# Kernel optimization log

Hardware: AMD Instinct MI355X
Metric: run time of the kernel (lower is better)

Reference implementation:

```python
import jax, jax.numpy as jnp
import numpy as np

D_MODEL = 1024
N_HEAD = 16
HEAD_DIM = D_MODEL // N_HEAD


def setup_inputs() -> dict:
    key = jax.random.key(0)
    ks = jax.random.split(key, 5)
    B, T = 2, 2048
    s = 1.0 / np.sqrt(D_MODEL)
    return {
        "x": jax.random.normal(ks[0], (B, T, D_MODEL), dtype=jnp.float32),
        "w_qkv": jax.random.normal(ks[1], (D_MODEL, 3 * D_MODEL), dtype=jnp.float32) * s,
        "b_qkv": jnp.zeros((3 * D_MODEL,), dtype=jnp.float32),
        "w_proj": jax.random.normal(ks[2], (D_MODEL, D_MODEL), dtype=jnp.float32) * s,
        "b_proj": jnp.zeros((D_MODEL,), dtype=jnp.float32),
    }


def reference(x, w_qkv, b_qkv, w_proj, b_proj):
    B, T, C = x.shape
    H, Dh = N_HEAD, HEAD_DIM
    scale = Dh ** -0.5
    qkv = x @ w_qkv + b_qkv                      # [B,T,3C]
    q, k, v = jnp.split(qkv, 3, axis=2)
    # [B,T,C] -> [B,H,T,Dh]
    q = q.reshape(B, T, H, Dh).transpose(0, 2, 1, 3)
    k = k.reshape(B, T, H, Dh).transpose(0, 2, 1, 3)
    v = v.reshape(B, T, H, Dh).transpose(0, 2, 1, 3)
    att = jnp.einsum("bhqd,bhkd->bhqk", q, k) * scale  # [B,H,T,T]
    causal = jnp.tril(jnp.ones((T, T), dtype=bool))
    att = jnp.where(causal, att, -jnp.inf)
    att = jax.nn.softmax(att, axis=-1)
    out = jnp.einsum("bhqk,bhkd->bhqd", att, v)  # [B,H,T,Dh]
    out = out.transpose(0, 2, 1, 3).reshape(B, T, C)
    return out @ w_proj + b_proj
```

## Files before the change

### kernel.cpp

```cpp
#include <hip/hip_runtime.h>
#include <hip/hip_bf16.h>

#define B_ 2
#define T_ 2048
#define C_ 1024
#define H_ 16
#define DH_ 64

typedef __attribute__((ext_vector_type(8))) short bf16x8;
typedef __attribute__((ext_vector_type(4))) float f32x4;
typedef __attribute__((ext_vector_type(4))) unsigned int u32x4;

#define DEVI static __device__ __forceinline__

DEVI unsigned short f2bf(float f) {
  unsigned int u = __float_as_uint(f);
  u = (u + 0x7fffu + ((u >> 16) & 1u)) >> 16;
  return (unsigned short)u;
}

DEVI f32x4 mfma16(bf16x8 a, bf16x8 b, f32x4 c) {
  return __builtin_amdgcn_mfma_f32_16x16x32_bf16(a, b, c, 0, 0, 0);
}

DEVI void gload_lds16(const unsigned short* g, unsigned short* l) {
  __builtin_amdgcn_global_load_lds(
      (const __attribute__((address_space(1))) unsigned int*)g,
      (__attribute__((address_space(3))) unsigned int*)l, 16, 0, 0);
}

DEVI unsigned int cvtpk_bf16(float lo, float hi) {
  unsigned int r;
  asm("v_cvt_pk_bf16_f32 %0, %1, %2" : "=v"(r) : "v"(lo), "v"(hi));
  return r;
}

DEVI int kperm(int kv) {
  return (kv & 3) | (((kv >> 3) & 1) << 2) | (((kv >> 5) & 1) << 3) |
         (((kv >> 2) & 1) << 4) | (((kv >> 4) & 1) << 5);
}

__global__ __launch_bounds__(256) void prep_kernel(
    const float* __restrict__ x, const float* __restrict__ w_qkv,
    const float* __restrict__ w_proj, unsigned short* __restrict__ xb,
    unsigned short* __restrict__ wqkvT, unsigned short* __restrict__ wprojT) {
  __shared__ float tile[32][33];
  int b = blockIdx.x, tid = threadIdx.x;
  if (b < 4096) {
    int i = b * 256 + tid;
    float4 v = reinterpret_cast<const float4*>(x)[i];
    ushort4 o;
    o.x = f2bf(v.x); o.y = f2bf(v.y); o.z = f2bf(v.z); o.w = f2bf(v.w);
    reinterpret_cast<ushort4*>(xb)[i] = o;
  } else {
    const float* in;
    unsigned short* out;
    int R, C, bb;
    if (b < 7168) { bb = b - 4096; in = w_qkv; out = wqkvT; R = 1024; C = 3072; }
    else          { bb = b - 7168; in = w_proj; out = wprojT; R = 1024; C = 1024; }
    int nbx = C >> 5;
    int c0 = (bb % nbx) * 32, r0 = (bb / nbx) * 32;
    int tx = tid & 31, ty = tid >> 5;
#pragma unroll
    for (int j = 0; j < 32; j += 8)
      tile[ty + j][tx] = in[(size_t)(r0 + ty + j) * C + c0 + tx];
    __syncthreads();
#pragma unroll
    for (int j = 0; j < 32; j += 8)
      out[(size_t)(c0 + ty + j) * R + r0 + tx] = f2bf(tile[tx][ty + j]);
  }
}

__global__ __launch_bounds__(256, 2) void gemm192_qkv(
    const unsigned short* __restrict__ A, const unsigned short* __restrict__ Bt,
    const float* __restrict__ bias,
    unsigned short* __restrict__ qbuf, unsigned short* __restrict__ kbuf,
    unsigned short* __restrict__ vtbuf) {
  __shared__ __attribute__((aligned(16))) unsigned short As[2][128 * 64];
  __shared__ __attribute__((aligned(16))) unsigned short Bs[2][192 * 64];
  const int Kd = 1024;
  int tid = threadIdx.x;
  int lane = tid & 63, w = tid >> 6;
  int wn = w;
  int lrow = lane & 15, lgrp = lane >> 4;

  int g = blockIdx.x;
  int gs = (g & 7) * 64 + (g >> 3);
  int by = gs >> 4, bx = gs & 15;
  int bm = by * 128, bn = bx * 192;
  const unsigned short* Ab = A + (size_t)bm * Kd;
  const unsigned short* Bb = Bt + (size_t)bn * Kd;

  int sL[2], scl[2];
#pragma unroll
  for (int it = 0; it < 2; ++it) {
    int c = tid + it * 256;
    int L = c >> 3, s = c & 7, v = s ^ (L & 7);
    sL[it] = L;
    scl[it] = (v >> 2) * 32 + (v & 3) * 8;
  }

  auto stgA = [&](int t, int h) {
    unsigned short* dst = As[t & 1] + h * 4096;
    int k0 = t << 6;
#pragma unroll
    for (int it = 0; it < 2; ++it)
      gload_lds16(Ab + (size_t)(h * 64 + sL[it]) * Kd + k0 + scl[it],
                  dst + (tid + it * 256) * 8);
  };
  auto stgB3 = [&](int t, int th) {
    unsigned short* dst = Bs[t & 1] + th * 4096;
    int k0 = t << 6;
#pragma unroll
    for (int it = 0; it < 2; ++it)
      gload_lds16(Bb + (size_t)(th * 64 + sL[it]) * Kd + k0 + scl[it],
                  dst + (tid + it * 256) * 8);
  };

  auto lda = [&](const unsigned short* buf, int mi, int kk) -> bf16x8 {
    int row = mi * 16 + lrow;
    int s = ((kk << 2) | lgrp) ^ (row & 7);
    return *reinterpret_cast<const bf16x8*>((const char*)buf + row * 128 + s * 16);
  };
  auto ldb = [&](const unsigned short* buf, int ni, int kk) -> bf16x8 {
    int row = wn * 48 + ni * 16 + lrow;
    int s = ((kk << 2) | lgrp) ^ (row & 7);
    return *reinterpret_cast<const bf16x8*>((const char*)buf + row * 128 + s * 16);
  };

  f32x4 acc[8][3] = {};
  bf16x8 bfr[3][2], af[2][2];

#define PHASE_TAIL                                          \
  __builtin_amdgcn_s_barrier();                             \
  __builtin_amdgcn_s_setprio(1);

#define MFMA_TRI(base)                                      \
  _Pragma("unroll") for (int ii = 0; ii < 2; ++ii)          \
  _Pragma("unroll") for (int ni = 0; ni < 3; ++ni) {        \
    acc[(base) + ii][ni] = mfma16(af[ii][0], bfr[ni][0], acc[(base) + ii][ni]); \
    acc[(base) + ii][ni] = mfma16(af[ii][1], bfr[ni][1], acc[(base) + ii][ni]); \
  }

#define PHASE_END                                           \
  __builtin_amdgcn_s_setprio(0);                            \
  __builtin_amdgcn_s_barrier();

  stgA(0, 0); stgA(0, 1);
  stgB3(0, 0); stgB3(0, 1); stgB3(0, 2);
  stgB3(1, 0); stgB3(1, 1); stgB3(1, 2);
  asm volatile("s_waitcnt vmcnt(6)" ::: "memory");
  __builtin_amdgcn_s_barrier();

#pragma unroll 1
  for (int j = 0; j < 8; ++j) {
    const bool nl = (j < 7);
    const int t1 = 2 * j + 1, t2 = 2 * j + 2, t3 = 2 * j + 3;

#pragma unroll
    for (int ni = 0; ni < 3; ++ni) { bfr[ni][0] = ldb(Bs[0], ni, 0); bfr[ni][1] = ldb(Bs[0], ni, 1); }
    af[0][0] = lda(As[0], 0, 0); af[0][1] = lda(As[0], 0, 1);
    af[1][0] = lda(As[0], 1, 0); af[1][1] = lda(As[0], 1, 1);
    stgA(t1, 0);
    PHASE_TAIL; MFMA_TRI(0); PHASE_END;

    af[0][0] = lda(As[0], 2, 0); af[0][1] = lda(As[0], 2, 1);
    af[1][0] = lda(As[0], 3, 0); af[1][1] = lda(As[0], 3, 1);
    stgA(t1, 1);
    if (nl) stgB3(t2, 0);
    PHASE_TAIL; MFMA_TRI(2); PHASE_END;

    af[0][0] = lda(As[0], 4, 0); af[0][1] = lda(As[0], 4, 1);
    af[1][0] = lda(As[0], 5, 0); af[1][1] = lda(As[0], 5, 1);
    if (nl) stgB3(t2, 1);
    PHASE_TAIL; MFMA_TRI(4); PHASE_END;

    af[0][0] = lda(As[0], 6, 0); af[0][1] = lda(As[0], 6, 1);
    af[1][0] = lda(As[0], 7, 0); af[1][1] = lda(As[0], 7, 1);
    if (nl) stgB3(t2, 2);
    PHASE_TAIL; MFMA_TRI(6);
    __builtin_amdgcn_s_setprio(0);
    if (nl) { asm volatile("s_waitcnt vmcnt(6)" ::: "memory"); }
    else    { asm volatile("s_waitcnt vmcnt(0)" ::: "memory"); }
    __builtin_amdgcn_s_barrier();

#pragma unroll
    for (int ni = 0; ni < 3; ++ni) { bfr[ni][0] = ldb(Bs[1], ni, 0); bfr[ni][1] = ldb(Bs[1], ni, 1); }
    af[0][0] = lda(As[1], 0, 0); af[0][1] = lda(As[1], 0, 1);
    af[1][0] = lda(As[1], 1, 0); af[1][1] = lda(As[1], 1, 1);
    if (nl) stgA(t2, 0);
    PHASE_TAIL; MFMA_TRI(0); PHASE_END;

    af[0][0] = lda(As[1], 2, 0); af[0][1] = lda(As[1], 2, 1);
    af[1][0] = lda(As[1], 3, 0); af[1][1] = lda(As[1], 3, 1);
    if (nl) { stgA(t2, 1); stgB3(t3, 0); }
    PHASE_TAIL; MFMA_TRI(2); PHASE_END;

    af[0][0] = lda(As[1], 4, 0); af[0][1] = lda(As[1], 4, 1);
    af[1][0] = lda(As[1], 5, 0); af[1][1] = lda(As[1], 5, 1);
    if (nl) stgB3(t3, 1);
    PHASE_TAIL; MFMA_TRI(4); PHASE_END;

    af[0][0] = lda(As[1], 6, 0); af[0][1] = lda(As[1], 6, 1);
    af[1][0] = lda(As[1], 7, 0); af[1][1] = lda(As[1], 7, 1);
    if (nl) stgB3(t3, 2);
    PHASE_TAIL; MFMA_TRI(6);
    __builtin_amdgcn_s_setprio(0);
    if (nl) { asm volatile("s_waitcnt vmcnt(6)" ::: "memory"); }
    __builtin_amdgcn_s_barrier();
  }
#undef PHASE_TAIL
#undef MFMA_TRI
#undef PHASE_END

  int c0 = bn + wn * 48;
#pragma unroll
  for (int ni = 0; ni < 3; ++ni) {
    int col = c0 + ni * 16 + lrow;
    float bv = bias[col];
    int which = col >> 10, cc = col & 1023;
    int h = cc >> 6, d = cc & 63;
#pragma unroll
    for (int mi = 0; mi < 8; ++mi) {
      int rowb = bm + mi * 16 + lgrp * 4;
      int b = rowb >> 11, tt = rowb & 2047;
      if (which == 2) {
        ushort4 pk;
        pk.x = f2bf(acc[mi][ni][0] + bv);
        pk.y = f2bf(acc[mi][ni][1] + bv);
        pk.z = f2bf(acc[mi][ni][2] + bv);
        pk.w = f2bf(acc[mi][ni][3] + bv);
        *reinterpret_cast<ushort4*>(vtbuf + ((size_t)((b * 16 + h) * 64 + d)) * T_ + tt) = pk;
      } else {
        unsigned short* dst = (which == 0) ? qbuf : kbuf;
        size_t base = ((size_t)(b * 16 + h) * T_ + tt) * DH_ + d;
#pragma unroll
        for (int r = 0; r < 4; ++r)
          dst[base + (size_t)r * DH_] = f2bf(acc[mi][ni][r] + bv);
      }
    }
  }
}

__global__ __launch_bounds__(256, 2) void gemm_proj(
    const unsigned short* __restrict__ A, const unsigned short* __restrict__ Bt,
    const float* __restrict__ bias, float* __restrict__ outp) {
  __shared__ __attribute__((aligned(16))) unsigned short As[2][128 * 64];
  __shared__ __attribute__((aligned(16))) unsigned short Bs[2][128 * 64];
  const int Kd = 1024, Nd = 1024;
  int tid = threadIdx.x;
  int lane = tid & 63, w = tid >> 6;
  int wn = w;
  int lrow = lane & 15, lgrp = lane >> 4;

  int g = blockIdx.x;
  int gs = (g & 7) * 32 + (g >> 3);
  int by = gs >> 3, bx = gs & 7;
  int bm = by * 128, bn = bx * 128;
  const unsigned short* Ab = A + (size_t)bm * Kd;
  const unsigned short* Bb = Bt + (size_t)bn * Kd;

  int sL[2], scl[2];
#pragma unroll
  for (int it = 0; it < 2; ++it) {
    int c = tid + it * 256;
    int L = c >> 3, s = c & 7, v = s ^ (L & 7);
    sL[it] = L;
    scl[it] = (v >> 2) * 32 + (v & 3) * 8;
  }

  auto stgA = [&](int t, int h) {
    unsigned short* dst = As[t & 1] + h * 4096;
    int k0 = t << 6;
#pragma unroll
    for (int it = 0; it < 2; ++it)
      gload_lds16(Ab + (size_t)(h * 64 + sL[it]) * Kd + k0 + scl[it],
                  dst + (tid + it * 256) * 8);
  };
  auto stgB = [&](int t, int h) {
    unsigned short* dst = Bs[t & 1] + h * 4096;
    int k0 = t << 6;
#pragma unroll
    for (int it = 0; it < 2; ++it)
      gload_lds16(Bb + (size_t)(h * 64 + sL[it]) * Kd + k0 + scl[it],
                  dst + (tid + it * 256) * 8);
  };

  auto lda = [&](const unsigned short* buf, int mi, int kk) -> bf16x8 {
    int row = mi * 16 + lrow;
    int s = ((kk << 2) | lgrp) ^ (row & 7);
    return *reinterpret_cast<const bf16x8*>((const char*)buf + row * 128 + s * 16);
  };
  auto ldb = [&](const unsigned short* buf, int ni, int kk) -> bf16x8 {
    int row = wn * 32 + ni * 16 + lrow;
    int s = ((kk << 2) | lgrp) ^ (row & 7);
    return *reinterpret_cast<const bf16x8*>((const char*)buf + row * 128 + s * 16);
  };

  f32x4 acc[8][2] = {};
  bf16x8 bfr[2][2], af[2][2];

#define PHASE_TAIL                                          \
  __builtin_amdgcn_s_barrier();                             \
  __builtin_amdgcn_s_setprio(1);

#define MFMA_DUO(base)                                      \
  _Pragma("unroll") for (int ii = 0; ii < 2; ++ii)          \
  _Pragma("unroll") for (int ni = 0; ni < 2; ++ni) {        \
    acc[(base) + ii][ni] = mfma16(af[ii][0], bfr[ni][0], acc[(base) + ii][ni]); \
    acc[(base) + ii][ni] = mfma16(af[ii][1], bfr[ni][1], acc[(base) + ii][ni]); \
  }

#define PHASE_END                                           \
  __builtin_amdgcn_s_setprio(0);                            \
  __builtin_amdgcn_s_barrier();

  stgA(0, 0); stgA(0, 1); stgB(0, 0); stgB(0, 1);
  stgB(1, 0); stgB(1, 1);
  asm volatile("s_waitcnt vmcnt(4)" ::: "memory");
  __builtin_amdgcn_s_barrier();

#pragma unroll 1
  for (int j = 0; j < 8; ++j) {
    const bool nl = (j < 7);
    const int t1 = 2 * j + 1, t2 = 2 * j + 2, t3 = 2 * j + 3;

#pragma unroll
    for (int ni = 0; ni < 2; ++ni) { bfr[ni][0] = ldb(Bs[0], ni, 0); bfr[ni][1] = ldb(Bs[0], ni, 1); }
    af[0][0] = lda(As[0], 0, 0); af[0][1] = lda(As[0], 0, 1);
    af[1][0] = lda(As[0], 1, 0); af[1][1] = lda(As[0], 1, 1);
    stgA(t1, 0);
    PHASE_TAIL; MFMA_DUO(0); PHASE_END;

    af[0][0] = lda(As[0], 2, 0); af[0][1] = lda(As[0], 2, 1);
    af[1][0] = lda(As[0], 3, 0); af[1][1] = lda(As[0], 3, 1);
    stgA(t1, 1);
    if (nl) stgB(t2, 0);
    PHASE_TAIL; MFMA_DUO(2); PHASE_END;

    af[0][0] = lda(As[0], 4, 0); af[0][1] = lda(As[0], 4, 1);
    af[1][0] = lda(As[0], 5, 0); af[1][1] = lda(As[0], 5, 1);
    if (nl) stgB(t2, 1);
    PHASE_TAIL; MFMA_DUO(4); PHASE_END;

    af[0][0] = lda(As[0], 6, 0); af[0][1] = lda(As[0], 6, 1);
    af[1][0] = lda(As[0], 7, 0); af[1][1] = lda(As[0], 7, 1);
    PHASE_TAIL; MFMA_DUO(6);
    __builtin_amdgcn_s_setprio(0);
    if (nl) { asm volatile("s_waitcnt vmcnt(4)" ::: "memory"); }
    else    { asm volatile("s_waitcnt vmcnt(0)" ::: "memory"); }
    __builtin_amdgcn_s_barrier();

#pragma unroll
    for (int ni = 0; ni < 2; ++ni) { bfr[ni][0] = ldb(Bs[1], ni, 0); bfr[ni][1] = ldb(Bs[1], ni, 1); }
    af[0][0] = lda(As[1], 0, 0); af[0][1] = lda(As[1], 0, 1);
    af[1][0] = lda(As[1], 1, 0); af[1][1] = lda(As[1], 1, 1);
    if (nl) stgA(t2, 0);
    PHASE_TAIL; MFMA_DUO(0); PHASE_END;

    af[0][0] = lda(As[1], 2, 0); af[0][1] = lda(As[1], 2, 1);
    af[1][0] = lda(As[1], 3, 0); af[1][1] = lda(As[1], 3, 1);
    if (nl) { stgA(t2, 1); stgB(t3, 0); }
    PHASE_TAIL; MFMA_DUO(2); PHASE_END;

    af[0][0] = lda(As[1], 4, 0); af[0][1] = lda(As[1], 4, 1);
    af[1][0] = lda(As[1], 5, 0); af[1][1] = lda(As[1], 5, 1);
    if (nl) stgB(t3, 1);
    PHASE_TAIL; MFMA_DUO(4); PHASE_END;

    af[0][0] = lda(As[1], 6, 0); af[0][1] = lda(As[1], 6, 1);
    af[1][0] = lda(As[1], 7, 0); af[1][1] = lda(As[1], 7, 1);
    PHASE_TAIL; MFMA_DUO(6);
    __builtin_amdgcn_s_setprio(0);
    if (nl) { asm volatile("s_waitcnt vmcnt(4)" ::: "memory"); }
    __builtin_amdgcn_s_barrier();
  }
#undef PHASE_TAIL
#undef MFMA_DUO
#undef PHASE_END

  int c0 = bn + wn * 32;
#pragma unroll
  for (int ni = 0; ni < 2; ++ni) {
    int col = c0 + ni * 16 + lrow;
    float bv = bias[col];
#pragma unroll
    for (int mi = 0; mi < 8; ++mi) {
      int rowb = bm + mi * 16 + lgrp * 4;
#pragma unroll
      for (int r = 0; r < 4; ++r)
        outp[(size_t)(rowb + r) * Nd + col] = acc[mi][ni][r] + bv;
    }
  }
}

__global__ __launch_bounds__(256, 4) void attn_kernel(
    const unsigned short* __restrict__ qbuf,
    const unsigned short* __restrict__ kbuf,
    const unsigned short* __restrict__ vtbuf,
    unsigned short* __restrict__ attno) {
  __shared__ __attribute__((aligned(16))) unsigned short Ks[64 * 64];
  __shared__ __attribute__((aligned(16))) unsigned short Vts[64 * 64];

  int tid = threadIdx.x;
  int lane = tid & 63, w = tid >> 6;
  int lrow = lane & 15, lgrp = lane >> 4;

  int g = blockIdx.x;
  int s = g >> 8;
  int p = (g >> 3) & 7;
  int bh = (g & 7) | (((g >> 6) & 3) << 3);
  int qb = (s == 0) ? p : (s == 1) ? (31 - p) : (s == 2) ? (8 + p) : (23 - p);
  int wq0 = qb * 64 + w * 16;
  int nkb = qb + 1;

  const unsigned short* Qb = qbuf + (size_t)bh * T_ * DH_;
  const unsigned short* Kb = kbuf + (size_t)bh * T_ * DH_;
  const unsigned short* Vb = vtbuf + (size_t)bh * DH_ * T_;

  int srow0 = tid >> 3, scol = tid & 7;
  int srow1 = srow0 + 32;
  int pk0 = kperm(srow0), pk1 = kperm(srow1);
  int soffK0 = pk0 * 128 + ((scol * 16) ^ ((pk0 & 7) << 4));
  int soffK1 = pk1 * 128 + ((scol * 16) ^ ((pk1 & 7) << 4));
  int soffV0 = srow0 * 128 + ((scol * 16) ^ ((srow0 & 7) << 4));
  int soffV1 = srow1 * 128 + ((scol * 16) ^ ((srow1 & 7) << 4));

  const float SC = 0.125f * 1.44269504f;
  int kvbase = ((lgrp & 1) << 3) | ((lgrp >> 1) << 5);
  const int koff[4] = {0, 4, 16, 20};

  bf16x8 qf[2];
#pragma unroll
  for (int ks = 0; ks < 2; ++ks)
    qf[ks] = *reinterpret_cast<const bf16x8*>(
        Qb + (size_t)(wq0 + lrow) * DH_ + ks * 32 + lgrp * 8);

  f32x4 o[4] = {};
  float l_run = 0.f;

  bf16x8 sk0, sk1, sv0, sv1;
  auto stage_load = [&](int kb) {
    sk0 = *reinterpret_cast<const bf16x8*>(Kb + (size_t)(kb * 64 + srow0) * DH_ + scol * 8);
    sk1 = *reinterpret_cast<const bf16x8*>(Kb + (size_t)(kb * 64 + srow1) * DH_ + scol * 8);
    sv0 = *reinterpret_cast<const bf16x8*>(Vb + (size_t)srow0 * T_ + kb * 64 + scol * 8);
    sv1 = *reinterpret_cast<const bf16x8*>(Vb + (size_t)srow1 * T_ + kb * 64 + scol * 8);
  };
  auto stage_write = [&]() {
    *reinterpret_cast<bf16x8*>((char*)Ks + soffK0) = sk0;
    *reinterpret_cast<bf16x8*>((char*)Ks + soffK1) = sk1;
    *reinterpret_cast<bf16x8*>((char*)Vts + soffV0) = sv0;
    *reinterpret_cast<bf16x8*>((char*)Vts + soffV1) = sv1;
  };

  stage_load(0);
#pragma unroll 1
  for (int kb = 0; kb < nkb; ++kb) {
    if (kb > 0) __syncthreads();
    stage_write();
    __syncthreads();
    if (kb + 1 < nkb) stage_load(kb + 1);

    f32x4 sreg[4] = {};
#pragma unroll
    for (int ks = 0; ks < 2; ++ks) {
      bf16x8 kf[4];
#pragma unroll
      for (int ni = 0; ni < 4; ++ni) {
        int kr = ni * 16 + lrow;
        int off = kr * 128 + (((ks * 32 + lgrp * 8) * 2) ^ ((kr & 7) << 4));
        kf[ni] = *reinterpret_cast<const bf16x8*>((const char*)Ks + off);
      }
      __builtin_amdgcn_s_setprio(1);
#pragma unroll
      for (int ni = 0; ni < 4; ++ni)
        sreg[ni] = mfma16(kf[ni], qf[ks], sreg[ni]);
      __builtin_amdgcn_s_setprio(0);
    }

    if (kb == qb) {
      int q = wq0 + lrow;
#pragma unroll
      for (int ni = 0; ni < 4; ++ni) {
        int kvb = kb * 64 + kvbase + koff[ni];
#pragma unroll
        for (int r = 0; r < 4; ++r)
          if (kvb + r > q) sreg[ni][r] = -1e30f;
      }
    }

    f32x4 e[4];
#pragma unroll
    for (int ni = 0; ni < 4; ++ni)
#pragma unroll
      for (int r = 0; r < 4; ++r)
        e[ni][r] = __builtin_amdgcn_exp2f(sreg[ni][r] * SC);

    f32x4 ts = (e[0] + e[1]) + (e[2] + e[3]);
    l_run += (ts[0] + ts[1]) + (ts[2] + ts[3]);

    unsigned int Aw[4], Bw[4];
    Aw[0] = cvtpk_bf16(e[0][0], e[0][1]); Aw[1] = cvtpk_bf16(e[0][2], e[0][3]);
    Aw[2] = cvtpk_bf16(e[1][0], e[1][1]); Aw[3] = cvtpk_bf16(e[1][2], e[1][3]);
    Bw[0] = cvtpk_bf16(e[2][0], e[2][1]); Bw[1] = cvtpk_bf16(e[2][2], e[2][3]);
    Bw[2] = cvtpk_bf16(e[3][0], e[3][1]); Bw[3] = cvtpk_bf16(e[3][2], e[3][3]);
    u32x4 p0v, p1v;
#pragma unroll
    for (int ww = 0; ww < 4; ++ww) {
      auto sw = __builtin_amdgcn_permlane32_swap(Aw[ww], Bw[ww], false, false);
      p0v[ww] = sw[0];
      p1v[ww] = sw[1];
    }
    bf16x8 pa[2];
    pa[0] = __builtin_bit_cast(bf16x8, p0v);
    pa[1] = __builtin_bit_cast(bf16x8, p1v);

#pragma unroll
    for (int ks = 0; ks < 2; ++ks) {
      bf16x8 vf[4];
#pragma unroll
      for (int di = 0; di < 4; ++di) {
        int vr = di * 16 + lrow;
        int off = vr * 128 + (((ks * 32 + lgrp * 8) * 2) ^ ((vr & 7) << 4));
        vf[di] = *reinterpret_cast<const bf16x8*>((const char*)Vts + off);
      }
      __builtin_amdgcn_s_setprio(1);
#pragma unroll
      for (int di = 0; di < 4; ++di)
        o[di] = mfma16(pa[ks], vf[di], o[di]);
      __builtin_amdgcn_s_setprio(0);
    }
  }

  float rs = l_run;
  rs += __shfl_xor(rs, 16);
  rs += __shfl_xor(rs, 32);
  float linv = 1.0f / rs;

  int b = bh >> 4, h = bh & 15;
  float lr[4];
#pragma unroll
  for (int r = 0; r < 4; ++r) lr[r] = __shfl(linv, lgrp * 4 + r);
#pragma unroll
  for (int r = 0; r < 4; ++r) {
    int q = wq0 + lgrp * 4 + r;
    size_t base = ((size_t)(b * T_ + q)) * C_ + h * 64 + lrow;
#pragma unroll
    for (int di = 0; di < 4; ++di)
      attno[base + (size_t)di * 16] = f2bf(o[di][r] * lr[r]);
  }
}

extern "C" void kernel_launch(void* const* d_in, const int* in_sizes, int n_in,
                              void* d_out, int out_size, void* d_ws, size_t ws_size,
                              hipStream_t stream) {
  const float* x      = (const float*)d_in[0];
  const float* w_qkv  = (const float*)d_in[1];
  const float* b_qkv  = (const float*)d_in[2];
  const float* w_proj = (const float*)d_in[3];
  const float* b_proj = (const float*)d_in[4];

  char* ws = (char*)d_ws;
  unsigned short* xb     = (unsigned short*)(ws + 0);
  unsigned short* wqkvT  = (unsigned short*)(ws + 8388608);
  unsigned short* wprojT = (unsigned short*)(ws + 14680064);
  unsigned short* qbuf   = (unsigned short*)(ws + 16777216);
  unsigned short* kbuf   = (unsigned short*)(ws + 25165824);
  unsigned short* vtbuf  = (unsigned short*)(ws + 33554432);
  unsigned short* attno  = (unsigned short*)(ws + 41943040);

  prep_kernel<<<8192, 256, 0, stream>>>(x, w_qkv, w_proj, xb, wqkvT, wprojT);
  gemm192_qkv<<<dim3(512), 256, 0, stream>>>(xb, wqkvT, b_qkv, qbuf, kbuf, vtbuf);
  attn_kernel<<<dim3(1024), 256, 0, stream>>>(qbuf, kbuf, vtbuf, attno);
  gemm_proj<<<dim3(256), 256, 0, stream>>>(attno, wprojT, b_proj, (float*)d_out);
}
```

Before: 91.89 us.

## Double-buffer attention K/V tiles with direct global-to-LDS loads

The attention kernel now stages K and V tiles straight into shared memory with global_load_lds, with source addresses chosen so the existing swizzle and K permutation land correctly. Two LDS buffers let the next tile load while the current one is computed. This drops the register round trip and one barrier per iteration. In exchange LDS use doubles, which may limit occupancy under the 4-blocks launch bound, and the inverse-permutation addressing must be exact.

```diff
diff --git a/kernel.cpp b/kernel.cpp
--- a/kernel.cpp
+++ b/kernel.cpp
@@ -38,6 +38,10 @@
 DEVI int kperm(int kv) {
   return (kv & 3) | (((kv >> 3) & 1) << 2) | (((kv >> 5) & 1) << 3) |
          (((kv >> 2) & 1) << 4) | (((kv >> 4) & 1) << 5);
+}
+DEVI int kperm_inv(int R) {
+  return (R & 3) | (((R >> 4) & 1) << 2) | (((R >> 2) & 1) << 3) |
+         (((R >> 5) & 1) << 4) | (((R >> 3) & 1) << 5);
 }
 
 __global__ __launch_bounds__(256) void prep_kernel(
@@ -399,8 +403,8 @@
     const unsigned short* __restrict__ kbuf,
     const unsigned short* __restrict__ vtbuf,
     unsigned short* __restrict__ attno) {
-  __shared__ __attribute__((aligned(16))) unsigned short Ks[64 * 64];
-  __shared__ __attribute__((aligned(16))) unsigned short Vts[64 * 64];
+  __shared__ __attribute__((aligned(16))) unsigned short Ks[2][64 * 64];
+  __shared__ __attribute__((aligned(16))) unsigned short Vts[2][64 * 64];
 
   int tid = threadIdx.x;
   int lane = tid & 63, w = tid >> 6;
@@ -418,13 +422,15 @@
   const unsigned short* Kb = kbuf + (size_t)bh * T_ * DH_;
   const unsigned short* Vb = vtbuf + (size_t)bh * DH_ * T_;
 
-  int srow0 = tid >> 3, scol = tid & 7;
-  int srow1 = srow0 + 32;
-  int pk0 = kperm(srow0), pk1 = kperm(srow1);
-  int soffK0 = pk0 * 128 + ((scol * 16) ^ ((pk0 & 7) << 4));
-  int soffK1 = pk1 * 128 + ((scol * 16) ^ ((pk1 & 7) << 4));
-  int soffV0 = srow0 * 128 + ((scol * 16) ^ ((srow0 & 7) << 4));
-  int soffV1 = srow1 * 128 + ((scol * 16) ^ ((srow1 & 7) << 4));
+  int kgo[2], vgo[2], cdst[2];
+#pragma unroll
+  for (int it = 0; it < 2; ++it) {
+    int c = w * 128 + it * 64 + lane;
+    int R = c >> 3, sw = c & 7;
+    kgo[it] = kperm_inv(R) * DH_ + (sw ^ (R & 7)) * 8;
+    vgo[it] = R * T_ + (sw ^ (R & 7)) * 8;
+    cdst[it] = c * 8;
+  }
 
   const float SC = 0.125f * 1.44269504f;
   int kvbase = ((lgrp & 1) << 3) | ((lgrp >> 1) << 5);
@@ -439,27 +445,24 @@
   f32x4 o[4] = {};
   float l_run = 0.f;
 
-  bf16x8 sk0, sk1, sv0, sv1;
-  auto stage_load = [&](int kb) {
-    sk0 = *reinterpret_cast<const bf16x8*>(Kb + (size_t)(kb * 64 + srow0) * DH_ + scol * 8);
-    sk1 = *reinterpret_cast<const bf16x8*>(Kb + (size_t)(kb * 64 + srow1) * DH_ + scol * 8);
-    sv0 = *reinterpret_cast<const bf16x8*>(Vb + (size_t)srow0 * T_ + kb * 64 + scol * 8);
-    sv1 = *reinterpret_cast<const bf16x8*>(Vb + (size_t)srow1 * T_ + kb * 64 + scol * 8);
-  };
-  auto stage_write = [&]() {
-    *reinterpret_cast<bf16x8*>((char*)Ks + soffK0) = sk0;
-    *reinterpret_cast<bf16x8*>((char*)Ks + soffK1) = sk1;
-    *reinterpret_cast<bf16x8*>((char*)Vts + soffV0) = sv0;
-    *reinterpret_cast<bf16x8*>((char*)Vts + soffV1) = sv1;
-  };
-
-  stage_load(0);
+  auto stage_issue = [&](int kb, int buf) {
+#pragma unroll
+    for (int it = 0; it < 2; ++it) {
+      gload_lds16(Kb + (size_t)kb * 64 * DH_ + kgo[it], Ks[buf] + cdst[it]);
+      gload_lds16(Vb + (size_t)kb * 64 + vgo[it], Vts[buf] + cdst[it]);
+    }
+  };
+
+  stage_issue(0, 0);
 #pragma unroll 1
   for (int kb = 0; kb < nkb; ++kb) {
-    if (kb > 0) __syncthreads();
-    stage_write();
+    int cur = kb & 1;
+    asm volatile("s_waitcnt vmcnt(0)" ::: "memory");
     __syncthreads();
-    if (kb + 1 < nkb) stage_load(kb + 1);
+    if (kb + 1 < nkb) stage_issue(kb + 1, cur ^ 1);
+
+    const char* kbase = (const char*)Ks[cur];
+    const char* vbase = (const char*)Vts[cur];
 
     f32x4 sreg[4] = {};
 #pragma unroll
@@ -469,7 +472,7 @@
       for (int ni = 0; ni < 4; ++ni) {
         int kr = ni * 16 + lrow;
         int off = kr * 128 + (((ks * 32 + lgrp * 8) * 2) ^ ((kr & 7) << 4));
-        kf[ni] = *reinterpret_cast<const bf16x8*>((const char*)Ks + off);
+        kf[ni] = *reinterpret_cast<const bf16x8*>(kbase + off);
       }
       __builtin_amdgcn_s_setprio(1);
 #pragma unroll
@@ -522,7 +525,7 @@
       for (int di = 0; di < 4; ++di) {
         int vr = di * 16 + lrow;
         int off = vr * 128 + (((ks * 32 + lgrp * 8) * 2) ^ ((vr & 7) << 4));
-        vf[di] = *reinterpret_cast<const bf16x8*>((const char*)Vts + off);
+        vf[di] = *reinterpret_cast<const bf16x8*>(vbase + off);
       }
       __builtin_amdgcn_s_setprio(1);
 #pragma unroll
```

New measurement: 95.72 us. +4.2%, slower.

## Use 128-query attention blocks with 8 waves sharing each K/V tile

Applied to the files above, without the earlier changes.

The attention kernel now launches 512 blocks of 512 threads, each covering 128 query rows with 8 waves, instead of 1024 blocks of 64 rows. Each K/V tile staged in shared memory is reused by twice as many waves, which halves global K/V traffic per query and cuts the number of blocks. The causal mask now applies per wave whenever the key tile reaches past that wave's first query row, so the waves in the lower half do extra masked work on the diagonal tiles. Occupancy per block changes and load balancing now pairs blocks p and 15-p.

```diff
diff --git a/kernel.cpp b/kernel.cpp
--- a/kernel.cpp
+++ b/kernel.cpp
@@ -394,7 +394,7 @@
   }
 }
 
-__global__ __launch_bounds__(256, 4) void attn_kernel(
+__global__ __launch_bounds__(512, 2) void attn_kernel(
     const unsigned short* __restrict__ qbuf,
     const unsigned short* __restrict__ kbuf,
     const unsigned short* __restrict__ vtbuf,
@@ -408,23 +408,21 @@
 
   int g = blockIdx.x;
   int s = g >> 8;
-  int p = (g >> 3) & 7;
-  int bh = (g & 7) | (((g >> 6) & 3) << 3);
-  int qb = (s == 0) ? p : (s == 1) ? (31 - p) : (s == 2) ? (8 + p) : (23 - p);
-  int wq0 = qb * 64 + w * 16;
-  int nkb = qb + 1;
+  int idx = g & 255;
+  int bh = idx & 31;
+  int pp = idx >> 5;
+  int p = s ? (15 - pp) : pp;
+  int wq0 = p * 128 + w * 16;
+  int nkb = 2 * p + 2;
 
   const unsigned short* Qb = qbuf + (size_t)bh * T_ * DH_;
   const unsigned short* Kb = kbuf + (size_t)bh * T_ * DH_;
   const unsigned short* Vb = vtbuf + (size_t)bh * DH_ * T_;
 
-  int srow0 = tid >> 3, scol = tid & 7;
-  int srow1 = srow0 + 32;
-  int pk0 = kperm(srow0), pk1 = kperm(srow1);
-  int soffK0 = pk0 * 128 + ((scol * 16) ^ ((pk0 & 7) << 4));
-  int soffK1 = pk1 * 128 + ((scol * 16) ^ ((pk1 & 7) << 4));
-  int soffV0 = srow0 * 128 + ((scol * 16) ^ ((srow0 & 7) << 4));
-  int soffV1 = srow1 * 128 + ((scol * 16) ^ ((srow1 & 7) << 4));
+  int srow = tid >> 3, scol = tid & 7;
+  int pkr = kperm(srow);
+  int soffK = pkr * 128 + ((scol * 16) ^ ((pkr & 7) << 4));
+  int soffV = srow * 128 + ((scol * 16) ^ ((srow & 7) << 4));
 
   const float SC = 0.125f * 1.44269504f;
   int kvbase = ((lgrp & 1) << 3) | ((lgrp >> 1) << 5);
@@ -439,18 +437,14 @@
   f32x4 o[4] = {};
   float l_run = 0.f;
 
-  bf16x8 sk0, sk1, sv0, sv1;
+  bf16x8 sk, sv;
   auto stage_load = [&](int kb) {
-    sk0 = *reinterpret_cast<const bf16x8*>(Kb + (size_t)(kb * 64 + srow0) * DH_ + scol * 8);
-    sk1 = *reinterpret_cast<const bf16x8*>(Kb + (size_t)(kb * 64 + srow1) * DH_ + scol * 8);
-    sv0 = *reinterpret_cast<const bf16x8*>(Vb + (size_t)srow0 * T_ + kb * 64 + scol * 8);
-    sv1 = *reinterpret_cast<const bf16x8*>(Vb + (size_t)srow1 * T_ + kb * 64 + scol * 8);
+    sk = *reinterpret_cast<const bf16x8*>(Kb + (size_t)(kb * 64 + srow) * DH_ + scol * 8);
+    sv = *reinterpret_cast<const bf16x8*>(Vb + (size_t)srow * T_ + kb * 64 + scol * 8);
   };
   auto stage_write = [&]() {
-    *reinterpret_cast<bf16x8*>((char*)Ks + soffK0) = sk0;
-    *reinterpret_cast<bf16x8*>((char*)Ks + soffK1) = sk1;
-    *reinterpret_cast<bf16x8*>((char*)Vts + soffV0) = sv0;
-    *reinterpret_cast<bf16x8*>((char*)Vts + soffV1) = sv1;
+    *reinterpret_cast<bf16x8*>((char*)Ks + soffK) = sk;
+    *reinterpret_cast<bf16x8*>((char*)Vts + soffV) = sv;
   };
 
   stage_load(0);
@@ -478,7 +472,7 @@
       __builtin_amdgcn_s_setprio(0);
     }
 
-    if (kb == qb) {
+    if (kb * 64 + 63 > wq0) {
       int q = wq0 + lrow;
 #pragma unroll
       for (int ni = 0; ni < 4; ++ni) {
@@ -571,6 +565,6 @@
 
   prep_kernel<<<8192, 256, 0, stream>>>(x, w_qkv, w_proj, xb, wqkvT, wprojT);
   gemm192_qkv<<<dim3(512), 256, 0, stream>>>(xb, wqkvT, b_qkv, qbuf, kbuf, vtbuf);
-  attn_kernel<<<dim3(1024), 256, 0, stream>>>(qbuf, kbuf, vtbuf, attno);
+  attn_kernel<<<dim3(512), 512, 0, stream>>>(qbuf, kbuf, vtbuf, attno);
   gemm_proj<<<dim3(256), 256, 0, stream>>>(attno, wprojT, b_proj, (float*)d_out);
 }
```

Result: no change. 91.29 us, median of 2 (-0.7%).
